# Kernel tuning notes

Measured on AMD Instinct MI355X. Metric: run time of the kernel, lower is better.

The kernel has to match this reference:

```python
import jax, jax.numpy as jnp
import numpy as np

BN_EPS = 1e-5
SAMPLE_KEY = jax.random.key(42)


def setup_inputs() -> dict:
    key = jax.random.key(0)
    ks = jax.random.split(key, 12)
    B, W, E = 524288, 8, 4
    D = W * E  # 32, input dim of fc1

    def lin(k, fan_in, fan_out):
        k1, k2 = jax.random.split(k)
        bound = 1.0 / np.sqrt(fan_in)
        w = jax.random.uniform(k1, (fan_in, fan_out), jnp.float32, -bound, bound)
        b = jax.random.uniform(k2, (fan_out,), jnp.float32, -bound, bound)
        return w, b

    W1, b1 = lin(ks[0], D, 50)
    W2, b2 = lin(ks[1], 50, 30)
    W3, b3 = lin(ks[2], 30, 20)
    W4, b4 = lin(ks[3], 20, 15)
    W5, b5 = lin(ks[4], 15, W)
    # BatchNorm affine params (eval mode, running_mean=0, running_var=1)
    g1, be1 = jnp.ones((50,), jnp.float32), jnp.zeros((50,), jnp.float32)
    g2, be2 = jnp.ones((30,), jnp.float32), jnp.zeros((30,), jnp.float32)
    g3, be3 = jnp.ones((20,), jnp.float32), jnp.zeros((20,), jnp.float32)
    events = jax.random.normal(ks[5], (B, W, E), jnp.float32)
    return {"events": events,
            "W1": W1, "b1": b1, "g1": g1, "be1": be1,
            "W2": W2, "b2": b2, "g2": g2, "be2": be2,
            "W3": W3, "b3": b3, "g3": g3, "be3": be3,
            "W4": W4, "b4": b4, "W5": W5, "b5": b5}


def _bn_eval(x, g, b):
    # eval-mode BatchNorm1d with running_mean=0, running_var=1
    return x * (g / jnp.sqrt(1.0 + BN_EPS)) + b


def _probs(events, W1, b1, g1, be1, W2, b2, g2, be2, W3, b3, g3, be3, W4, b4, W5, b5):
    B = events.shape[0]
    x = events.reshape(B, -1)  # (B, window*event_size)
    h = jax.nn.relu(_bn_eval(x @ W1 + b1, g1, be1))
    h = jax.nn.relu(_bn_eval(h @ W2 + b2, g2, be2))
    h = jax.nn.relu(_bn_eval(h @ W3 + b3, g3, be3))
    h = jax.nn.relu(h @ W4 + b4)
    return jax.nn.sigmoid(h @ W5 + b5)  # (B, window_size)


def reference(events, W1, b1, g1, be1, W2, b2, g2, be2, W3, b3, g3, be3, W4, b4, W5, b5):
    p = _probs(events, W1, b1, g1, be1, W2, b2, g2, be2, W3, b3, g3, be3, W4, b4, W5, b5)
    # np.random.choice([0,1], p=[p, 1-p]) => P(choice=1) = 1 - p
    choice = jax.random.bernoulli(SAMPLE_KEY, 1.0 - p).astype(p.dtype)  # (B, W)
    chosen_events_np = 1.0 - choice
    flipped = jnp.abs(choice - p)            # prob of sampled outcome per element
    log_prob = jnp.log(jnp.prod(flipped, axis=1))  # (B,)
    return chosen_events_np, log_prob
```

## Files before the change

### kernel.cpp

```cpp
#include <hip/hip_runtime.h>
#include <math.h>

#define THREADS 256
#define P_MARGIN 1e-4f

__device__ __forceinline__ void tf2x32(unsigned x0, unsigned x1,
                                       unsigned &o0, unsigned &o1) {
  const unsigned k0 = 0u;
  const unsigned k1 = 42u;
  const unsigned k2 = 0x1BD11BDAu ^ k0 ^ k1;
  x0 += k0; x1 += k1;
#define TF_R(r) { x0 += x1; x1 = (x1 << (r)) | (x1 >> (32 - (r))); x1 ^= x0; }
  TF_R(13) TF_R(15) TF_R(26) TF_R(6)
  x0 += k1; x1 += k2 + 1u;
  TF_R(17) TF_R(29) TF_R(16) TF_R(24)
  x0 += k2; x1 += k0 + 2u;
  TF_R(13) TF_R(15) TF_R(26) TF_R(6)
  x0 += k0; x1 += k1 + 3u;
  TF_R(17) TF_R(29) TF_R(16) TF_R(24)
  x0 += k1; x1 += k2 + 4u;
  TF_R(13) TF_R(15) TF_R(26) TF_R(6)
  x0 += k2; x1 += k0 + 5u;
#undef TF_R
  o0 = x0; o1 = x1;
}

__global__ __launch_bounds__(THREADS, 4)
void wtf_fast_kernel(const float* __restrict__ events,
                     const float* __restrict__ W1, const float* __restrict__ b1,
                     const float* __restrict__ g1, const float* __restrict__ be1,
                     const float* __restrict__ W2, const float* __restrict__ b2,
                     const float* __restrict__ g2, const float* __restrict__ be2,
                     const float* __restrict__ W3, const float* __restrict__ b3,
                     const float* __restrict__ g3, const float* __restrict__ be3,
                     const float* __restrict__ W4, const float* __restrict__ b4,
                     const float* __restrict__ W5, const float* __restrict__ b5,
                     float* __restrict__ out_chosen,
                     float* __restrict__ out_logp,
                     unsigned* __restrict__ fixlist,
                     unsigned fixcap,
                     int B) {
  const int b = blockIdx.x * THREADS + threadIdx.x;
  if (b >= B) return;

  const float rden = (float)(1.0 / sqrt(1.0 + 1e-5));

  float x[32];
  const float4* ev4 = reinterpret_cast<const float4*>(events) + (size_t)b * 8;
#pragma unroll
  for (int q = 0; q < 8; ++q) {
    float4 v = ev4[q];
    x[4 * q + 0] = v.x; x[4 * q + 1] = v.y; x[4 * q + 2] = v.z; x[4 * q + 3] = v.w;
  }

  float a1[50];
#pragma unroll
  for (int n = 0; n < 50; ++n) a1[n] = b1[n];
#pragma unroll
  for (int k = 0; k < 32; ++k) {
    const float xk = x[k];
#pragma unroll
    for (int n = 0; n < 50; ++n) a1[n] = fmaf(xk, W1[k * 50 + n], a1[n]);
  }
#pragma unroll
  for (int n = 0; n < 50; ++n) {
    float s = fmaf(a1[n], g1[n] * rden, be1[n]);
    a1[n] = fmaxf(s, 0.f);
  }

  float a2[30];
#pragma unroll
  for (int n = 0; n < 30; ++n) a2[n] = b2[n];
#pragma unroll
  for (int k = 0; k < 50; ++k) {
    const float ak = a1[k];
#pragma unroll
    for (int n = 0; n < 30; ++n) a2[n] = fmaf(ak, W2[k * 30 + n], a2[n]);
  }
#pragma unroll
  for (int n = 0; n < 30; ++n) {
    float s = fmaf(a2[n], g2[n] * rden, be2[n]);
    a2[n] = fmaxf(s, 0.f);
  }

  float a3[20];
#pragma unroll
  for (int n = 0; n < 20; ++n) a3[n] = b3[n];
#pragma unroll
  for (int k = 0; k < 30; ++k) {
    const float ak = a2[k];
#pragma unroll
    for (int n = 0; n < 20; ++n) a3[n] = fmaf(ak, W3[k * 20 + n], a3[n]);
  }
#pragma unroll
  for (int n = 0; n < 20; ++n) {
    float s = fmaf(a3[n], g3[n] * rden, be3[n]);
    a3[n] = fmaxf(s, 0.f);
  }

  float a4[15];
#pragma unroll
  for (int n = 0; n < 15; ++n) a4[n] = b4[n];
#pragma unroll
  for (int k = 0; k < 20; ++k) {
    const float ak = a3[k];
#pragma unroll
    for (int n = 0; n < 15; ++n) a4[n] = fmaf(ak, W4[k * 15 + n], a4[n]);
  }
#pragma unroll
  for (int n = 0; n < 15; ++n) a4[n] = fmaxf(a4[n], 0.f);

  float p[8];
#pragma unroll
  for (int n = 0; n < 8; ++n) p[n] = b5[n];
#pragma unroll
  for (int k = 0; k < 15; ++k) {
    const float ak = a4[k];
#pragma unroll
    for (int n = 0; n < 8; ++n) p[n] = fmaf(ak, W5[k * 8 + n], p[n]);
  }
#pragma unroll
  for (int n = 0; n < 8; ++n) p[n] = 1.f / (1.f + expf(-p[n]));

  bool need = false;
  float prod = 1.f;
  float ch[8];
#pragma unroll
  for (int w = 0; w < 8; ++w) {
    unsigned j = 8u * (unsigned)b + (unsigned)w, o0, o1;
    tf2x32(0u, j, o0, o1);
    unsigned bits = o0 ^ o1;
    float u = __uint_as_float(0x3F800000u | (bits >> 9)) - 1.f;
    float thr = 1.f - p[w];
    bool choice = u < thr;
    need = need || (fabsf(u - thr) < P_MARGIN);
    ch[w] = choice ? 0.f : 1.f;
    prod *= choice ? thr : p[w];
  }
  if (need) {
    unsigned i = atomicAdd(&fixlist[0], 1u);
    if (i < fixcap) fixlist[1 + i] = (unsigned)b;
  }

  float4* oc = reinterpret_cast<float4*>(out_chosen) + (size_t)b * 2;
  oc[0] = make_float4(ch[0], ch[1], ch[2], ch[3]);
  oc[1] = make_float4(ch[4], ch[5], ch[6], ch[7]);
  out_logp[b] = logf(prod);
}

__global__ __launch_bounds__(64, 4)
void wtf_fix_kernel(const float* __restrict__ events,
                    const float* __restrict__ W1, const float* __restrict__ b1,
                    const float* __restrict__ g1, const float* __restrict__ be1,
                    const float* __restrict__ W2, const float* __restrict__ b2,
                    const float* __restrict__ g2, const float* __restrict__ be2,
                    const float* __restrict__ W3, const float* __restrict__ b3,
                    const float* __restrict__ g3, const float* __restrict__ be3,
                    const float* __restrict__ W4, const float* __restrict__ b4,
                    const float* __restrict__ W5, const float* __restrict__ b5,
                    float* __restrict__ out_chosen,
                    float* __restrict__ out_logp,
                    const unsigned* __restrict__ fixlist,
                    unsigned fixcap,
                    int B) {
  const unsigned raw = fixlist[0];
  const unsigned cnt = raw < fixcap ? raw : fixcap;
  if (blockIdx.x >= cnt) return;

  __shared__ double sA[64];
  __shared__ double sB[64];
  __shared__ double sF[8];

  const int t = threadIdx.x;
  const double denom = sqrt(1.0 + 1e-5);

  for (unsigned idx = blockIdx.x; idx < cnt; idx += gridDim.x) {
    const int b = (int)fixlist[1 + idx];

    if (t < 32) sA[t] = (double)events[(size_t)b * 32 + t];
    __syncthreads();

    double v = 0.0;
    if (t < 50) {
#pragma unroll
      for (int k = 0; k < 32; ++k) v = fma(sA[k], (double)W1[k * 50 + t], v);
      v += (double)b1[t];
      v = v * ((double)g1[t] / denom) + (double)be1[t];
      v = v > 0.0 ? v : 0.0;
    }
    __syncthreads();
    if (t < 50) sB[t] = v;
    __syncthreads();

    v = 0.0;
    if (t < 30) {
#pragma unroll
      for (int k = 0; k < 50; ++k) v = fma(sB[k], (double)W2[k * 30 + t], v);
      v += (double)b2[t];
      v = v * ((double)g2[t] / denom) + (double)be2[t];
      v = v > 0.0 ? v : 0.0;
    }
    __syncthreads();
    if (t < 30) sA[t] = v;
    __syncthreads();

    v = 0.0;
    if (t < 20) {
#pragma unroll
      for (int k = 0; k < 30; ++k) v = fma(sA[k], (double)W3[k * 20 + t], v);
      v += (double)b3[t];
      v = v * ((double)g3[t] / denom) + (double)be3[t];
      v = v > 0.0 ? v : 0.0;
    }
    __syncthreads();
    if (t < 20) sB[t] = v;
    __syncthreads();

    v = 0.0;
    if (t < 15) {
#pragma unroll
      for (int k = 0; k < 20; ++k) v = fma(sB[k], (double)W4[k * 15 + t], v);
      v += (double)b4[t];
      v = v > 0.0 ? v : 0.0;
    }
    __syncthreads();
    if (t < 15) sA[t] = v;
    __syncthreads();

    if (t < 8) {
      v = 0.0;
#pragma unroll
      for (int k = 0; k < 15; ++k) v = fma(sA[k], (double)W5[k * 8 + t], v);
      v += (double)b5[t];
      double p = 1.0 / (1.0 + exp(-v));
      unsigned j = 8u * (unsigned)b + (unsigned)t, o0, o1;
      tf2x32(0u, j, o0, o1);
      unsigned bits = o0 ^ o1;
      float u = __uint_as_float(0x3F800000u | (bits >> 9)) - 1.f;
      double thr = 1.0 - p;
      bool choice = ((double)u < thr);
      out_chosen[(size_t)b * 8 + t] = choice ? 0.f : 1.f;
      sF[t] = choice ? thr : p;
    }
    __syncthreads();
    if (t == 0) {
      double prod = 1.0;
      for (int w = 0; w < 8; ++w) prod *= sF[w];
      out_logp[b] = (float)log(prod);
    }
    __syncthreads();
  }
}

extern "C" void kernel_launch(void* const* d_in, const int* in_sizes, int n_in,
                              void* d_out, int out_size, void* d_ws, size_t ws_size,
                              hipStream_t stream) {
  const float* events = (const float*)d_in[0];
  const float* W1  = (const float*)d_in[1];
  const float* b1  = (const float*)d_in[2];
  const float* g1  = (const float*)d_in[3];
  const float* be1 = (const float*)d_in[4];
  const float* W2  = (const float*)d_in[5];
  const float* b2  = (const float*)d_in[6];
  const float* g2  = (const float*)d_in[7];
  const float* be2 = (const float*)d_in[8];
  const float* W3  = (const float*)d_in[9];
  const float* b3  = (const float*)d_in[10];
  const float* g3  = (const float*)d_in[11];
  const float* be3 = (const float*)d_in[12];
  const float* W4  = (const float*)d_in[13];
  const float* b4  = (const float*)d_in[14];
  const float* W5  = (const float*)d_in[15];
  const float* b5  = (const float*)d_in[16];

  const int B = in_sizes[0] / 32;
  float* out = (float*)d_out;
  float* out_chosen = out;
  float* out_logp   = out + (size_t)B * 8;
  unsigned* fixlist = (unsigned*)d_ws;
  unsigned fixcap = (unsigned)(ws_size / sizeof(unsigned) - 1);
  if (fixcap > (unsigned)B) fixcap = (unsigned)B;

  hipMemsetAsync(d_ws, 0, sizeof(unsigned), stream);

  const int blocks = (B + THREADS - 1) / THREADS;
  hipLaunchKernelGGL(wtf_fast_kernel, dim3(blocks), dim3(THREADS), 0, stream,
                     events, W1, b1, g1, be1, W2, b2, g2, be2,
                     W3, b3, g3, be3, W4, b4, W5, b5,
                     out_chosen, out_logp, fixlist, fixcap, B);
  hipLaunchKernelGGL(wtf_fix_kernel, dim3(1024), dim3(64), 0, stream,
                     events, W1, b1, g1, be1, W2, b2, g2, be2,
                     W3, b3, g3, be3, W4, b4, W5, b5,
                     out_chosen, out_logp, fixlist, fixcap, B);
}
```

Measured before the change: 237.9 us.

## Fuse fix-up pass into main kernel and use packed float2 FMAs

```diff
diff --git a/kernel.cpp b/kernel.cpp
--- a/kernel.cpp
+++ b/kernel.cpp
@@ -3,6 +3,9 @@
 
 #define THREADS 256
 #define P_MARGIN 1e-4f
+#define FIXCAP 32
+
+typedef float v2f __attribute__((ext_vector_type(2)));
 
 __device__ __forceinline__ void tf2x32(unsigned x0, unsigned x1,
                                        unsigned &o0, unsigned &o1) {
@@ -26,158 +29,176 @@
 }
 
 __global__ __launch_bounds__(THREADS, 4)
-void wtf_fast_kernel(const float* __restrict__ events,
-                     const float* __restrict__ W1, const float* __restrict__ b1,
-                     const float* __restrict__ g1, const float* __restrict__ be1,
-                     const float* __restrict__ W2, const float* __restrict__ b2,
-                     const float* __restrict__ g2, const float* __restrict__ be2,
-                     const float* __restrict__ W3, const float* __restrict__ b3,
-                     const float* __restrict__ g3, const float* __restrict__ be3,
-                     const float* __restrict__ W4, const float* __restrict__ b4,
-                     const float* __restrict__ W5, const float* __restrict__ b5,
-                     float* __restrict__ out_chosen,
-                     float* __restrict__ out_logp,
-                     unsigned* __restrict__ fixlist,
-                     unsigned fixcap,
-                     int B) {
-  const int b = blockIdx.x * THREADS + threadIdx.x;
-  if (b >= B) return;
-
-  const float rden = (float)(1.0 / sqrt(1.0 + 1e-5));
-
-  float x[32];
-  const float4* ev4 = reinterpret_cast<const float4*>(events) + (size_t)b * 8;
-#pragma unroll
-  for (int q = 0; q < 8; ++q) {
-    float4 v = ev4[q];
-    x[4 * q + 0] = v.x; x[4 * q + 1] = v.y; x[4 * q + 2] = v.z; x[4 * q + 3] = v.w;
-  }
-
-  float a1[50];
-#pragma unroll
-  for (int n = 0; n < 50; ++n) a1[n] = b1[n];
-#pragma unroll
-  for (int k = 0; k < 32; ++k) {
-    const float xk = x[k];
-#pragma unroll
-    for (int n = 0; n < 50; ++n) a1[n] = fmaf(xk, W1[k * 50 + n], a1[n]);
-  }
-#pragma unroll
-  for (int n = 0; n < 50; ++n) {
-    float s = fmaf(a1[n], g1[n] * rden, be1[n]);
-    a1[n] = fmaxf(s, 0.f);
-  }
-
-  float a2[30];
-#pragma unroll
-  for (int n = 0; n < 30; ++n) a2[n] = b2[n];
-#pragma unroll
-  for (int k = 0; k < 50; ++k) {
-    const float ak = a1[k];
-#pragma unroll
-    for (int n = 0; n < 30; ++n) a2[n] = fmaf(ak, W2[k * 30 + n], a2[n]);
-  }
-#pragma unroll
-  for (int n = 0; n < 30; ++n) {
-    float s = fmaf(a2[n], g2[n] * rden, be2[n]);
-    a2[n] = fmaxf(s, 0.f);
-  }
-
-  float a3[20];
-#pragma unroll
-  for (int n = 0; n < 20; ++n) a3[n] = b3[n];
-#pragma unroll
-  for (int k = 0; k < 30; ++k) {
-    const float ak = a2[k];
-#pragma unroll
-    for (int n = 0; n < 20; ++n) a3[n] = fmaf(ak, W3[k * 20 + n], a3[n]);
-  }
-#pragma unroll
-  for (int n = 0; n < 20; ++n) {
-    float s = fmaf(a3[n], g3[n] * rden, be3[n]);
-    a3[n] = fmaxf(s, 0.f);
-  }
-
-  float a4[15];
-#pragma unroll
-  for (int n = 0; n < 15; ++n) a4[n] = b4[n];
-#pragma unroll
-  for (int k = 0; k < 20; ++k) {
-    const float ak = a3[k];
-#pragma unroll
-    for (int n = 0; n < 15; ++n) a4[n] = fmaf(ak, W4[k * 15 + n], a4[n]);
-  }
-#pragma unroll
-  for (int n = 0; n < 15; ++n) a4[n] = fmaxf(a4[n], 0.f);
-
-  float p[8];
-#pragma unroll
-  for (int n = 0; n < 8; ++n) p[n] = b5[n];
-#pragma unroll
-  for (int k = 0; k < 15; ++k) {
-    const float ak = a4[k];
-#pragma unroll
-    for (int n = 0; n < 8; ++n) p[n] = fmaf(ak, W5[k * 8 + n], p[n]);
-  }
-#pragma unroll
-  for (int n = 0; n < 8; ++n) p[n] = 1.f / (1.f + expf(-p[n]));
-
-  bool need = false;
-  float prod = 1.f;
-  float ch[8];
-#pragma unroll
-  for (int w = 0; w < 8; ++w) {
-    unsigned j = 8u * (unsigned)b + (unsigned)w, o0, o1;
-    tf2x32(0u, j, o0, o1);
-    unsigned bits = o0 ^ o1;
-    float u = __uint_as_float(0x3F800000u | (bits >> 9)) - 1.f;
-    float thr = 1.f - p[w];
-    bool choice = u < thr;
-    need = need || (fabsf(u - thr) < P_MARGIN);
-    ch[w] = choice ? 0.f : 1.f;
-    prod *= choice ? thr : p[w];
-  }
-  if (need) {
-    unsigned i = atomicAdd(&fixlist[0], 1u);
-    if (i < fixcap) fixlist[1 + i] = (unsigned)b;
-  }
-
-  float4* oc = reinterpret_cast<float4*>(out_chosen) + (size_t)b * 2;
-  oc[0] = make_float4(ch[0], ch[1], ch[2], ch[3]);
-  oc[1] = make_float4(ch[4], ch[5], ch[6], ch[7]);
-  out_logp[b] = logf(prod);
-}
-
-__global__ __launch_bounds__(64, 4)
-void wtf_fix_kernel(const float* __restrict__ events,
-                    const float* __restrict__ W1, const float* __restrict__ b1,
-                    const float* __restrict__ g1, const float* __restrict__ be1,
-                    const float* __restrict__ W2, const float* __restrict__ b2,
-                    const float* __restrict__ g2, const float* __restrict__ be2,
-                    const float* __restrict__ W3, const float* __restrict__ b3,
-                    const float* __restrict__ g3, const float* __restrict__ be3,
-                    const float* __restrict__ W4, const float* __restrict__ b4,
-                    const float* __restrict__ W5, const float* __restrict__ b5,
-                    float* __restrict__ out_chosen,
-                    float* __restrict__ out_logp,
-                    const unsigned* __restrict__ fixlist,
-                    unsigned fixcap,
-                    int B) {
-  const unsigned raw = fixlist[0];
-  const unsigned cnt = raw < fixcap ? raw : fixcap;
-  if (blockIdx.x >= cnt) return;
-
+void wtf_kernel(const float* __restrict__ events,
+                const float* __restrict__ W1, const float* __restrict__ b1,
+                const float* __restrict__ g1, const float* __restrict__ be1,
+                const float* __restrict__ W2, const float* __restrict__ b2,
+                const float* __restrict__ g2, const float* __restrict__ be2,
+                const float* __restrict__ W3, const float* __restrict__ b3,
+                const float* __restrict__ g3, const float* __restrict__ be3,
+                const float* __restrict__ W4, const float* __restrict__ b4,
+                const float* __restrict__ W5, const float* __restrict__ b5,
+                float* __restrict__ out_chosen,
+                float* __restrict__ out_logp,
+                int B) {
+  __shared__ unsigned s_cnt;
+  __shared__ unsigned s_rows[FIXCAP];
   __shared__ double sA[64];
   __shared__ double sB[64];
   __shared__ double sF[8];
 
   const int t = threadIdx.x;
+  if (t == 0) s_cnt = 0;
+  __syncthreads();
+
+  const int b = blockIdx.x * THREADS + t;
+  const bool active = (b < B);
+  const float rden = (float)(1.0 / sqrt(1.0 + 1e-5));
+
+  if (active) {
+    float x[32];
+    const float4* ev4 = reinterpret_cast<const float4*>(events) + (size_t)b * 8;
+#pragma unroll
+    for (int q = 0; q < 8; ++q) {
+      float4 v = ev4[q];
+      x[4 * q + 0] = v.x; x[4 * q + 1] = v.y; x[4 * q + 2] = v.z; x[4 * q + 3] = v.w;
+    }
+
+    v2f A[25];
+#pragma unroll
+    for (int j = 0; j < 25; ++j) A[j] = v2f{b1[2 * j], b1[2 * j + 1]};
+#pragma unroll
+    for (int k = 0; k < 32; ++k) {
+      const v2f xk2 = {x[k], x[k]};
+#pragma unroll
+      for (int j = 0; j < 25; ++j) {
+        v2f w = {W1[k * 50 + 2 * j], W1[k * 50 + 2 * j + 1]};
+        A[j] = __builtin_elementwise_fma(xk2, w, A[j]);
+      }
+    }
+    float a1[50];
+#pragma unroll
+    for (int j = 0; j < 25; ++j) {
+      a1[2 * j + 0] = fmaxf(fmaf(A[j].x, g1[2 * j + 0] * rden, be1[2 * j + 0]), 0.f);
+      a1[2 * j + 1] = fmaxf(fmaf(A[j].y, g1[2 * j + 1] * rden, be1[2 * j + 1]), 0.f);
+    }
+
+    v2f C[15];
+#pragma unroll
+    for (int j = 0; j < 15; ++j) C[j] = v2f{b2[2 * j], b2[2 * j + 1]};
+#pragma unroll
+    for (int k = 0; k < 50; ++k) {
+      const v2f hk2 = {a1[k], a1[k]};
+#pragma unroll
+      for (int j = 0; j < 15; ++j) {
+        v2f w = {W2[k * 30 + 2 * j], W2[k * 30 + 2 * j + 1]};
+        C[j] = __builtin_elementwise_fma(hk2, w, C[j]);
+      }
+    }
+    float a2[30];
+#pragma unroll
+    for (int j = 0; j < 15; ++j) {
+      a2[2 * j + 0] = fmaxf(fmaf(C[j].x, g2[2 * j + 0] * rden, be2[2 * j + 0]), 0.f);
+      a2[2 * j + 1] = fmaxf(fmaf(C[j].y, g2[2 * j + 1] * rden, be2[2 * j + 1]), 0.f);
+    }
+
+    v2f D[10];
+#pragma unroll
+    for (int j = 0; j < 10; ++j) D[j] = v2f{b3[2 * j], b3[2 * j + 1]};
+#pragma unroll
+    for (int k = 0; k < 30; ++k) {
+      const v2f hk2 = {a2[k], a2[k]};
+#pragma unroll
+      for (int j = 0; j < 10; ++j) {
+        v2f w = {W3[k * 20 + 2 * j], W3[k * 20 + 2 * j + 1]};
+        D[j] = __builtin_elementwise_fma(hk2, w, D[j]);
+      }
+    }
+    float a3[20];
+#pragma unroll
+    for (int j = 0; j < 10; ++j) {
+      a3[2 * j + 0] = fmaxf(fmaf(D[j].x, g3[2 * j + 0] * rden, be3[2 * j + 0]), 0.f);
+      a3[2 * j + 1] = fmaxf(fmaf(D[j].y, g3[2 * j + 1] * rden, be3[2 * j + 1]), 0.f);
+    }
+
+    v2f E[7];
+    float e14 = b4[14];
+#pragma unroll
+    for (int j = 0; j < 7; ++j) E[j] = v2f{b4[2 * j], b4[2 * j + 1]};
+#pragma unroll
+    for (int k = 0; k < 20; ++k) {
+      const float hk = a3[k];
+      const v2f hk2 = {hk, hk};
+#pragma unroll
+      for (int j = 0; j < 7; ++j) {
+        v2f w = {W4[k * 15 + 2 * j], W4[k * 15 + 2 * j + 1]};
+        E[j] = __builtin_elementwise_fma(hk2, w, E[j]);
+      }
+      e14 = fmaf(hk, W4[k * 15 + 14], e14);
+    }
+    float a4[15];
+#pragma unroll
+    for (int j = 0; j < 7; ++j) {
+      a4[2 * j + 0] = fmaxf(E[j].x, 0.f);
+      a4[2 * j + 1] = fmaxf(E[j].y, 0.f);
+    }
+    a4[14] = fmaxf(e14, 0.f);
+
+    v2f P[4];
+#pragma unroll
+    for (int j = 0; j < 4; ++j) P[j] = v2f{b5[2 * j], b5[2 * j + 1]};
+#pragma unroll
+    for (int k = 0; k < 15; ++k) {
+      const v2f hk2 = {a4[k], a4[k]};
+#pragma unroll
+      for (int j = 0; j < 4; ++j) {
+        v2f w = {W5[k * 8 + 2 * j], W5[k * 8 + 2 * j + 1]};
+        P[j] = __builtin_elementwise_fma(hk2, w, P[j]);
+      }
+    }
+    float p[8];
+#pragma unroll
+    for (int j = 0; j < 4; ++j) {
+      p[2 * j + 0] = 1.f / (1.f + expf(-P[j].x));
+      p[2 * j + 1] = 1.f / (1.f + expf(-P[j].y));
+    }
+
+    bool need = false;
+    float prod = 1.f;
+    float ch[8];
+#pragma unroll
+    for (int w = 0; w < 8; ++w) {
+      unsigned j = 8u * (unsigned)b + (unsigned)w, o0, o1;
+      tf2x32(0u, j, o0, o1);
+      unsigned bits = o0 ^ o1;
+      float u = __uint_as_float(0x3F800000u | (bits >> 9)) - 1.f;
+      float thr = 1.f - p[w];
+      bool choice = u < thr;
+      need = need || (fabsf(u - thr) < P_MARGIN);
+      ch[w] = choice ? 0.f : 1.f;
+      prod *= choice ? thr : p[w];
+    }
+    if (need) {
+      unsigned i = atomicAdd(&s_cnt, 1u);
+      if (i < FIXCAP) s_rows[i] = (unsigned)b;
+    }
+
+    float4* oc = reinterpret_cast<float4*>(out_chosen) + (size_t)b * 2;
+    oc[0] = make_float4(ch[0], ch[1], ch[2], ch[3]);
+    oc[1] = make_float4(ch[4], ch[5], ch[6], ch[7]);
+    out_logp[b] = logf(prod);
+  }
+
+  __syncthreads();
+  unsigned cnt = s_cnt;
+  if (cnt > FIXCAP) cnt = FIXCAP;
+  if (cnt == 0) return;
+
   const double denom = sqrt(1.0 + 1e-5);
-
-  for (unsigned idx = blockIdx.x; idx < cnt; idx += gridDim.x) {
-    const int b = (int)fixlist[1 + idx];
-
-    if (t < 32) sA[t] = (double)events[(size_t)b * 32 + t];
+  for (unsigned r = 0; r < cnt; ++r) {
+    const int rb = (int)s_rows[r];
+
+    if (t < 32) sA[t] = (double)events[(size_t)rb * 32 + t];
     __syncthreads();
 
     double v = 0.0;
@@ -233,20 +254,20 @@
       for (int k = 0; k < 15; ++k) v = fma(sA[k], (double)W5[k * 8 + t], v);
       v += (double)b5[t];
       double p = 1.0 / (1.0 + exp(-v));
-      unsigned j = 8u * (unsigned)b + (unsigned)t, o0, o1;
+      unsigned j = 8u * (unsigned)rb + (unsigned)t, o0, o1;
       tf2x32(0u, j, o0, o1);
       unsigned bits = o0 ^ o1;
       float u = __uint_as_float(0x3F800000u | (bits >> 9)) - 1.f;
       double thr = 1.0 - p;
       bool choice = ((double)u < thr);
-      out_chosen[(size_t)b * 8 + t] = choice ? 0.f : 1.f;
+      out_chosen[(size_t)rb * 8 + t] = choice ? 0.f : 1.f;
       sF[t] = choice ? thr : p;
     }
     __syncthreads();
     if (t == 0) {
       double prod = 1.0;
       for (int w = 0; w < 8; ++w) prod *= sF[w];
-      out_logp[b] = (float)log(prod);
+      out_logp[rb] = (float)log(prod);
     }
     __syncthreads();
   }
@@ -277,19 +298,10 @@
   float* out = (float*)d_out;
   float* out_chosen = out;
   float* out_logp   = out + (size_t)B * 8;
-  unsigned* fixlist = (unsigned*)d_ws;
-  unsigned fixcap = (unsigned)(ws_size / sizeof(unsigned) - 1);
-  if (fixcap > (unsigned)B) fixcap = (unsigned)B;
-
-  hipMemsetAsync(d_ws, 0, sizeof(unsigned), stream);
 
   const int blocks = (B + THREADS - 1) / THREADS;
-  hipLaunchKernelGGL(wtf_fast_kernel, dim3(blocks), dim3(THREADS), 0, stream,
+  hipLaunchKernelGGL(wtf_kernel, dim3(blocks), dim3(THREADS), 0, stream,
                      events, W1, b1, g1, be1, W2, b2, g2, be2,
                      W3, b3, g3, be3, W4, b4, W5, b5,
-                     out_chosen, out_logp, fixlist, fixcap, B);
-  hipLaunchKernelGGL(wtf_fix_kernel, dim3(1024), dim3(64), 0, stream,
-                     events, W1, b1, g1, be1, W2, b2, g2, be2,
-                     W3, b3, g3, be3, W4, b4, W5, b5,
-                     out_chosen, out_logp, fixlist, fixcap, B);
+                     out_chosen, out_logp, B);
 }
```

Result: no change. 234.2 us (-1.6%).

## Fuse fast MLP pass and double-precision fixup into one kernel with block-local fixlist

Applied to the files above, without the earlier changes.

```diff
diff --git a/kernel.cpp b/kernel.cpp
--- a/kernel.cpp
+++ b/kernel.cpp
@@ -3,6 +3,7 @@
 
 #define THREADS 256
 #define P_MARGIN 1e-4f
+#define FIXCAP 32
 
 __device__ __forceinline__ void tf2x32(unsigned x0, unsigned x1,
                                        unsigned &o0, unsigned &o1) {
@@ -25,159 +26,147 @@
   o0 = x0; o1 = x1;
 }
 
-__global__ __launch_bounds__(THREADS, 4)
-void wtf_fast_kernel(const float* __restrict__ events,
-                     const float* __restrict__ W1, const float* __restrict__ b1,
-                     const float* __restrict__ g1, const float* __restrict__ be1,
-                     const float* __restrict__ W2, const float* __restrict__ b2,
-                     const float* __restrict__ g2, const float* __restrict__ be2,
-                     const float* __restrict__ W3, const float* __restrict__ b3,
-                     const float* __restrict__ g3, const float* __restrict__ be3,
-                     const float* __restrict__ W4, const float* __restrict__ b4,
-                     const float* __restrict__ W5, const float* __restrict__ b5,
-                     float* __restrict__ out_chosen,
-                     float* __restrict__ out_logp,
-                     unsigned* __restrict__ fixlist,
-                     unsigned fixcap,
-                     int B) {
-  const int b = blockIdx.x * THREADS + threadIdx.x;
-  if (b >= B) return;
-
-  const float rden = (float)(1.0 / sqrt(1.0 + 1e-5));
-
-  float x[32];
-  const float4* ev4 = reinterpret_cast<const float4*>(events) + (size_t)b * 8;
-#pragma unroll
-  for (int q = 0; q < 8; ++q) {
-    float4 v = ev4[q];
-    x[4 * q + 0] = v.x; x[4 * q + 1] = v.y; x[4 * q + 2] = v.z; x[4 * q + 3] = v.w;
-  }
-
-  float a1[50];
-#pragma unroll
-  for (int n = 0; n < 50; ++n) a1[n] = b1[n];
-#pragma unroll
-  for (int k = 0; k < 32; ++k) {
-    const float xk = x[k];
-#pragma unroll
-    for (int n = 0; n < 50; ++n) a1[n] = fmaf(xk, W1[k * 50 + n], a1[n]);
-  }
-#pragma unroll
-  for (int n = 0; n < 50; ++n) {
-    float s = fmaf(a1[n], g1[n] * rden, be1[n]);
-    a1[n] = fmaxf(s, 0.f);
-  }
-
-  float a2[30];
-#pragma unroll
-  for (int n = 0; n < 30; ++n) a2[n] = b2[n];
-#pragma unroll
-  for (int k = 0; k < 50; ++k) {
-    const float ak = a1[k];
-#pragma unroll
-    for (int n = 0; n < 30; ++n) a2[n] = fmaf(ak, W2[k * 30 + n], a2[n]);
-  }
-#pragma unroll
-  for (int n = 0; n < 30; ++n) {
-    float s = fmaf(a2[n], g2[n] * rden, be2[n]);
-    a2[n] = fmaxf(s, 0.f);
-  }
-
-  float a3[20];
-#pragma unroll
-  for (int n = 0; n < 20; ++n) a3[n] = b3[n];
-#pragma unroll
-  for (int k = 0; k < 30; ++k) {
-    const float ak = a2[k];
-#pragma unroll
-    for (int n = 0; n < 20; ++n) a3[n] = fmaf(ak, W3[k * 20 + n], a3[n]);
-  }
-#pragma unroll
-  for (int n = 0; n < 20; ++n) {
-    float s = fmaf(a3[n], g3[n] * rden, be3[n]);
-    a3[n] = fmaxf(s, 0.f);
-  }
-
-  float a4[15];
-#pragma unroll
-  for (int n = 0; n < 15; ++n) a4[n] = b4[n];
-#pragma unroll
-  for (int k = 0; k < 20; ++k) {
-    const float ak = a3[k];
-#pragma unroll
-    for (int n = 0; n < 15; ++n) a4[n] = fmaf(ak, W4[k * 15 + n], a4[n]);
-  }
-#pragma unroll
-  for (int n = 0; n < 15; ++n) a4[n] = fmaxf(a4[n], 0.f);
-
-  float p[8];
-#pragma unroll
-  for (int n = 0; n < 8; ++n) p[n] = b5[n];
-#pragma unroll
-  for (int k = 0; k < 15; ++k) {
-    const float ak = a4[k];
-#pragma unroll
-    for (int n = 0; n < 8; ++n) p[n] = fmaf(ak, W5[k * 8 + n], p[n]);
-  }
-#pragma unroll
-  for (int n = 0; n < 8; ++n) p[n] = 1.f / (1.f + expf(-p[n]));
-
-  bool need = false;
-  float prod = 1.f;
-  float ch[8];
-#pragma unroll
-  for (int w = 0; w < 8; ++w) {
-    unsigned j = 8u * (unsigned)b + (unsigned)w, o0, o1;
-    tf2x32(0u, j, o0, o1);
-    unsigned bits = o0 ^ o1;
-    float u = __uint_as_float(0x3F800000u | (bits >> 9)) - 1.f;
-    float thr = 1.f - p[w];
-    bool choice = u < thr;
-    need = need || (fabsf(u - thr) < P_MARGIN);
-    ch[w] = choice ? 0.f : 1.f;
-    prod *= choice ? thr : p[w];
-  }
-  if (need) {
-    unsigned i = atomicAdd(&fixlist[0], 1u);
-    if (i < fixcap) fixlist[1 + i] = (unsigned)b;
-  }
-
-  float4* oc = reinterpret_cast<float4*>(out_chosen) + (size_t)b * 2;
-  oc[0] = make_float4(ch[0], ch[1], ch[2], ch[3]);
-  oc[1] = make_float4(ch[4], ch[5], ch[6], ch[7]);
-  out_logp[b] = logf(prod);
-}
-
-__global__ __launch_bounds__(64, 4)
-void wtf_fix_kernel(const float* __restrict__ events,
-                    const float* __restrict__ W1, const float* __restrict__ b1,
-                    const float* __restrict__ g1, const float* __restrict__ be1,
-                    const float* __restrict__ W2, const float* __restrict__ b2,
-                    const float* __restrict__ g2, const float* __restrict__ be2,
-                    const float* __restrict__ W3, const float* __restrict__ b3,
-                    const float* __restrict__ g3, const float* __restrict__ be3,
-                    const float* __restrict__ W4, const float* __restrict__ b4,
-                    const float* __restrict__ W5, const float* __restrict__ b5,
-                    float* __restrict__ out_chosen,
-                    float* __restrict__ out_logp,
-                    const unsigned* __restrict__ fixlist,
-                    unsigned fixcap,
-                    int B) {
-  const unsigned raw = fixlist[0];
-  const unsigned cnt = raw < fixcap ? raw : fixcap;
-  if (blockIdx.x >= cnt) return;
-
+__global__ __launch_bounds__(THREADS, 8)
+void wtf_kernel(const float* __restrict__ events,
+                const float* __restrict__ W1, const float* __restrict__ b1,
+                const float* __restrict__ g1, const float* __restrict__ be1,
+                const float* __restrict__ W2, const float* __restrict__ b2,
+                const float* __restrict__ g2, const float* __restrict__ be2,
+                const float* __restrict__ W3, const float* __restrict__ b3,
+                const float* __restrict__ g3, const float* __restrict__ be3,
+                const float* __restrict__ W4, const float* __restrict__ b4,
+                const float* __restrict__ W5, const float* __restrict__ b5,
+                float* __restrict__ out_chosen,
+                float* __restrict__ out_logp,
+                int B) {
+  __shared__ unsigned s_cnt;
+  __shared__ unsigned s_rows[FIXCAP];
   __shared__ double sA[64];
   __shared__ double sB[64];
   __shared__ double sF[8];
 
   const int t = threadIdx.x;
+  if (t == 0) s_cnt = 0;
+  __syncthreads();
+
+  const int b = blockIdx.x * THREADS + t;
+  const bool active = (b < B);
+  const float rden = (float)(1.0 / sqrt(1.0 + 1e-5));
+
+  if (active) {
+    float x[32];
+    const float4* ev4 = reinterpret_cast<const float4*>(events) + (size_t)b * 8;
+#pragma unroll
+    for (int q = 0; q < 8; ++q) {
+      float4 v = ev4[q];
+      x[4 * q + 0] = v.x; x[4 * q + 1] = v.y; x[4 * q + 2] = v.z; x[4 * q + 3] = v.w;
+    }
+
+    float a1[50];
+#pragma unroll
+    for (int n = 0; n < 50; ++n) a1[n] = b1[n];
+#pragma unroll
+    for (int k = 0; k < 32; ++k) {
+      const float xk = x[k];
+#pragma unroll
+      for (int n = 0; n < 50; ++n) a1[n] = fmaf(xk, W1[k * 50 + n], a1[n]);
+    }
+#pragma unroll
+    for (int n = 0; n < 50; ++n) {
+      float s = fmaf(a1[n], g1[n] * rden, be1[n]);
+      a1[n] = fmaxf(s, 0.f);
+    }
+
+    float a2[30];
+#pragma unroll
+    for (int n = 0; n < 30; ++n) a2[n] = b2[n];
+#pragma unroll
+    for (int k = 0; k < 50; ++k) {
+      const float ak = a1[k];
+#pragma unroll
+      for (int n = 0; n < 30; ++n) a2[n] = fmaf(ak, W2[k * 30 + n], a2[n]);
+    }
+#pragma unroll
+    for (int n = 0; n < 30; ++n) {
+      float s = fmaf(a2[n], g2[n] * rden, be2[n]);
+      a2[n] = fmaxf(s, 0.f);
+    }
+
+    float a3[20];
+#pragma unroll
+    for (int n = 0; n < 20; ++n) a3[n] = b3[n];
+#pragma unroll
+    for (int k = 0; k < 30; ++k) {
+      const float ak = a2[k];
+#pragma unroll
+      for (int n = 0; n < 20; ++n) a3[n] = fmaf(ak, W3[k * 20 + n], a3[n]);
+    }
+#pragma unroll
+    for (int n = 0; n < 20; ++n) {
+      float s = fmaf(a3[n], g3[n] * rden, be3[n]);
+      a3[n] = fmaxf(s, 0.f);
+    }
+
+    float a4[15];
+#pragma unroll
+    for (int n = 0; n < 15; ++n) a4[n] = b4[n];
+#pragma unroll
+    for (int k = 0; k < 20; ++k) {
+      const float ak = a3[k];
+#pragma unroll
+      for (int n = 0; n < 15; ++n) a4[n] = fmaf(ak, W4[k * 15 + n], a4[n]);
+    }
+#pragma unroll
+    for (int n = 0; n < 15; ++n) a4[n] = fmaxf(a4[n], 0.f);
+
+    float p[8];
+#pragma unroll
+    for (int n = 0; n < 8; ++n) p[n] = b5[n];
+#pragma unroll
+    for (int k = 0; k < 15; ++k) {
+      const float ak = a4[k];
+#pragma unroll
+      for (int n = 0; n < 8; ++n) p[n] = fmaf(ak, W5[k * 8 + n], p[n]);
+    }
+#pragma unroll
+    for (int n = 0; n < 8; ++n) p[n] = 1.f / (1.f + expf(-p[n]));
+
+    bool need = false;
+    float prod = 1.f;
+    float ch[8];
+#pragma unroll
+    for (int w = 0; w < 8; ++w) {
+      unsigned j = 8u * (unsigned)b + (unsigned)w, o0, o1;
+      tf2x32(0u, j, o0, o1);
+      unsigned bits = o0 ^ o1;
+      float u = __uint_as_float(0x3F800000u | (bits >> 9)) - 1.f;
+      float thr = 1.f - p[w];
+      bool choice = u < thr;
+      need = need || (fabsf(u - thr) < P_MARGIN);
+      ch[w] = choice ? 0.f : 1.f;
+      prod *= choice ? thr : p[w];
+    }
+    if (need) {
+      unsigned i = atomicAdd(&s_cnt, 1u);
+      if (i < FIXCAP) s_rows[i] = (unsigned)b;
+    }
+
+    float4* oc = reinterpret_cast<float4*>(out_chosen) + (size_t)b * 2;
+    oc[0] = make_float4(ch[0], ch[1], ch[2], ch[3]);
+    oc[1] = make_float4(ch[4], ch[5], ch[6], ch[7]);
+    out_logp[b] = logf(prod);
+  }
+
+  __syncthreads();
+  unsigned cnt = s_cnt;
+  if (cnt > FIXCAP) cnt = FIXCAP;
+  if (cnt == 0) return;
+
   const double denom = sqrt(1.0 + 1e-5);
-
-  for (unsigned idx = blockIdx.x; idx < cnt; idx += gridDim.x) {
-    const int b = (int)fixlist[1 + idx];
-
-    if (t < 32) sA[t] = (double)events[(size_t)b * 32 + t];
+  for (unsigned r = 0; r < cnt; ++r) {
+    const int rb = (int)s_rows[r];
+
+    if (t < 32) sA[t] = (double)events[(size_t)rb * 32 + t];
     __syncthreads();
 
     double v = 0.0;
@@ -233,20 +222,20 @@
       for (int k = 0; k < 15; ++k) v = fma(sA[k], (double)W5[k * 8 + t], v);
       v += (double)b5[t];
       double p = 1.0 / (1.0 + exp(-v));
-      unsigned j = 8u * (unsigned)b + (unsigned)t, o0, o1;
+      unsigned j = 8u * (unsigned)rb + (unsigned)t, o0, o1;
       tf2x32(0u, j, o0, o1);
       unsigned bits = o0 ^ o1;
       float u = __uint_as_float(0x3F800000u | (bits >> 9)) - 1.f;
       double thr = 1.0 - p;
       bool choice = ((double)u < thr);
-      out_chosen[(size_t)b * 8 + t] = choice ? 0.f : 1.f;
+      out_chosen[(size_t)rb * 8 + t] = choice ? 0.f : 1.f;
       sF[t] = choice ? thr : p;
     }
     __syncthreads();
     if (t == 0) {
       double prod = 1.0;
       for (int w = 0; w < 8; ++w) prod *= sF[w];
-      out_logp[b] = (float)log(prod);
+      out_logp[rb] = (float)log(prod);
     }
     __syncthreads();
   }
@@ -277,19 +266,10 @@
   float* out = (float*)d_out;
   float* out_chosen = out;
   float* out_logp   = out + (size_t)B * 8;
-  unsigned* fixlist = (unsigned*)d_ws;
-  unsigned fixcap = (unsigned)(ws_size / sizeof(unsigned) - 1);
-  if (fixcap > (unsigned)B) fixcap = (unsigned)B;
-
-  hipMemsetAsync(d_ws, 0, sizeof(unsigned), stream);
 
   const int blocks = (B + THREADS - 1) / THREADS;
-  hipLaunchKernelGGL(wtf_fast_kernel, dim3(blocks), dim3(THREADS), 0, stream,
+  hipLaunchKernelGGL(wtf_kernel, dim3(blocks), dim3(THREADS), 0, stream,
                      events, W1, b1, g1, be1, W2, b2, g2, be2,
                      W3, b3, g3, be3, W4, b4, W5, b5,
-                     out_chosen, out_logp, fixlist, fixcap, B);
-  hipLaunchKernelGGL(wtf_fix_kernel, dim3(1024), dim3(64), 0, stream,
-                     events, W1, b1, g1, be1, W2, b2, g2, be2,
-                     W3, b3, g3, be3, W4, b4, W5, b5,
-                     out_chosen, out_logp, fixlist, fixcap, B);
+                     out_chosen, out_logp, B);
 }
```

Result: slower. 295.0 us (+24.0%).
